# Kernel optimization log

Hardware: AMD Instinct MI355X
Metric: run time of the kernel (lower is better)

Reference implementation:

```python
import jax, jax.numpy as jnp
import numpy as np

B, V, CIN, H, W = 2, 4, 256, 96, 96
COUT, VS = 32, 64


def setup_inputs() -> dict:
    key = jax.random.key(0)
    k1, k2, k3, k4, k5 = jax.random.split(key, 5)
    features = jax.random.normal(k1, (B, V, CIN, H, W), dtype=jnp.float32)
    proj_matricies = jax.random.normal(k2, (B, V, 3, 4), dtype=jnp.float32)
    coord_volumes = jax.random.normal(k3, (B, VS, VS, VS, 3), dtype=jnp.float32) * 1000.0
    W_proc = jax.random.normal(k4, (COUT, CIN), dtype=jnp.float32) * 0.05
    b_proc = jax.random.normal(k5, (COUT,), dtype=jnp.float32) * 0.01
    return {"features": features, "proj_matricies": proj_matricies,
            "coord_volumes": coord_volumes, "W_proc": W_proc, "b_proc": b_proc}


def _bilinear_sample(feat, x, y):
    # feat: [C, H, W]; x, y: [N] pixel coords (align_corners=True mapping already applied)
    Hh, Ww = feat.shape[1], feat.shape[2]
    x0 = jnp.floor(x).astype(jnp.int32); x1 = x0 + 1
    y0 = jnp.floor(y).astype(jnp.int32); y1 = y0 + 1
    wx1 = x - x0; wx0 = 1.0 - wx1
    wy1 = y - y0; wy0 = 1.0 - wy1

    def gather(xi, yi):
        valid = ((xi >= 0) & (xi < Ww) & (yi >= 0) & (yi < Hh)).astype(feat.dtype)
        xc = jnp.clip(xi, 0, Ww - 1); yc = jnp.clip(yi, 0, Hh - 1)
        return feat[:, yc, xc] * valid  # [C, N] (zeros padding)

    return (gather(x0, y0) * (wx0 * wy0)
            + gather(x1, y0) * (wx1 * wy0)
            + gather(x0, y1) * (wx0 * wy1)
            + gather(x1, y1) * (wx1 * wy1))


def reference(features, proj_matricies, coord_volumes, W_proc, b_proc):
    b, v, cin, h, w = features.shape
    vs = coord_volumes.shape[1]
    # 1x1 conv (process_feature)
    feats = jnp.einsum('bvchw,oc->bvohw', features, W_proc) + b_proc[None, None, :, None, None]
    c = feats.shape[2]
    # homogeneous 3D grid points: [B, N, 4]
    pts = coord_volumes.reshape(b, -1, 3)
    pts_h = jnp.concatenate([pts, jnp.ones(pts.shape[:-1] + (1,), pts.dtype)], axis=-1)
    # project to image plane: [B, V, N, 3] homogeneous (u, v, w)
    proj_pts = jnp.einsum('bvij,bnj->bvni', proj_matricies, pts_h)
    wz = proj_pts[..., 2]
    invalid = wz <= 0.0
    wz_safe = jnp.where(wz == 0.0, 1.0, wz)
    u = proj_pts[..., 0] / wz_safe
    ve = proj_pts[..., 1] / wz_safe
    # normalized grid coords (faithful to original: x divided by feature_shape[0]=H, y by feature_shape[1]=W)
    gx = 2.0 * (u / h - 0.5)
    gy = 2.0 * (ve / w - 0.5)
    # align_corners=True pixel coords: x indexes width, y indexes height
    px = (gx + 1.0) * 0.5 * (w - 1)
    py = (gy + 1.0) * 0.5 * (h - 1)
    # sample per (batch, view): [B, V, C, N]
    sampled = jax.vmap(jax.vmap(_bilinear_sample))(feats, px, py)
    sampled = jnp.where(invalid[:, :, None, :], 0.0, sampled)
    # softmax over views per (b, c, voxel), weighted sum
    weights = jax.nn.softmax(sampled, axis=1)
    vol = jnp.sum(sampled * weights, axis=1)  # [B, C, N]
    return vol.reshape(b, c, vs, vs, vs)
```

## Files before the change

kernel.cpp:

```cpp
#include <hip/hip_runtime.h>
#include <hip/hip_bf16.h>

#define CIN   256
#define COUT  32
#define IMG_H 96
#define IMG_W 96
#define HW    (IMG_H*IMG_W)
#define NB    2
#define NV    4
#define VSZ   64
#define NVOX  (VSZ*VSZ*VSZ)

typedef __attribute__((ext_vector_type(2))) float f32x2;

__device__ __forceinline__ float fast_exp2(float x) {
    float r;
    asm("v_exp_f32 %0, %1" : "=v"(r) : "v"(x));
    return r;
}

__global__ __launch_bounds__(512) void conv1x1_kernel(
    const float* __restrict__ features,
    const float* __restrict__ Wp,
    const float* __restrict__ bp,
    __hip_bfloat16* __restrict__ out)
{
    __shared__ float red[2][COUT][128];
    const int wid  = threadIdx.x >> 6;
    const int pxs  = __builtin_amdgcn_readfirstlane(wid & 1);
    const int og   = __builtin_amdgcn_readfirstlane((wid >> 1) & 1);
    const int kh   = __builtin_amdgcn_readfirstlane(wid >> 2);
    const int lane = threadIdx.x & 63;
    const int pxl  = pxs*64 + lane;
    const int bv   = blockIdx.y;
    const int px   = blockIdx.x*128 + pxl;
    const float* f     = features + (size_t)bv*CIN*HW + (size_t)kh*128*HW + px;
    const float* wbase = Wp + (size_t)og*16*CIN + kh*128;

    float acc[16];
    #pragma unroll
    for (int j = 0; j < 16; ++j) acc[j] = 0.f;

    for (int cc = 0; cc < 128; cc += 8) {
        float x[8];
        #pragma unroll
        for (int i = 0; i < 8; ++i)
            x[i] = f[(size_t)(cc + i)*HW];
        #pragma unroll
        for (int i = 0; i < 8; ++i) {
            #pragma unroll
            for (int j = 0; j < 16; ++j)
                acc[j] += x[i] * wbase[(size_t)j*CIN + cc + i];
        }
    }

    #pragma unroll
    for (int j = 0; j < 16; ++j)
        red[kh][og*16 + j][pxl] = acc[j];
    __syncthreads();

    if (kh == 0) {
        union { uint4 u4[2]; __hip_bfloat16 hh[16]; } pk;
        #pragma unroll
        for (int j = 0; j < 16; ++j) {
            const int ch = og*16 + j;
            pk.hh[j] = __float2bfloat16(red[0][ch][pxl] + red[1][ch][pxl] + bp[ch]);
        }
        __hip_bfloat16* op = out + (size_t)(bv*HW + px)*COUT + og*16;
        *(uint4*)(op)     = pk.u4[0];
        *(uint4*)(op + 8) = pk.u4[1];
    }
}

__global__ __launch_bounds__(256, 4) void volgen_kernel(
    const __hip_bfloat16* __restrict__ feats,
    const float* __restrict__ proj,
    const float* __restrict__ coords,
    float* __restrict__ out)
{
    const int tid = threadIdx.x;
    const int b   = blockIdx.y;
    const int n   = blockIdx.x*256 + tid;

    const float* cp = coords + ((size_t)b*NVOX + n)*3;
    const float X = cp[0], Y = cp[1], Z = cp[2];

    const float LOG2E = 1.4426950408889634f;

    int   off[NV][4];
    float wgt[NV][4];
    #pragma unroll
    for (int v = 0; v < NV; ++v) {
        const float* P = proj + (size_t)(b*NV + v)*12;
        const float wz = P[8]*X + P[9]*Y + P[10]*Z + P[11];
        const bool  vz = wz > 0.f;
        const float rz = __builtin_amdgcn_rcpf(wz);
        float px = (P[0]*X + P[1]*Y + P[2]*Z + P[3]) * rz * (95.f/96.f);
        float py = (P[4]*X + P[5]*Y + P[6]*Z + P[7]) * rz * (95.f/96.f);
        px = vz ? px : 0.f;  py = vz ? py : 0.f;
        px = fminf(fmaxf(px, -1.0e6f), 1.0e6f);
        py = fminf(fmaxf(py, -1.0e6f), 1.0e6f);
        const float fx0 = floorf(px), fy0 = floorf(py);
        const int x0 = (int)fx0, y0 = (int)fy0, x1 = x0+1, y1 = y0+1;
        const float wx1 = px - fx0, wx0 = 1.f - wx1;
        const float wy1 = py - fy0, wy0 = 1.f - wy1;
        const bool vx0 = (unsigned)x0 < (unsigned)IMG_W;
        const bool vx1 = (unsigned)x1 < (unsigned)IMG_W;
        const bool vy0 = (unsigned)y0 < (unsigned)IMG_H;
        const bool vy1 = (unsigned)y1 < (unsigned)IMG_H;
        const int cx0 = min(max(x0, 0), IMG_W-1), cx1 = min(max(x1, 0), IMG_W-1);
        const int cy0 = min(max(y0, 0), IMG_H-1), cy1 = min(max(y1, 0), IMG_H-1);
        const int base = ((b*NV + v)*HW)*COUT*2;
        off[v][0] = base + (cy0*IMG_W + cx0)*(COUT*2);  wgt[v][0] = (vz & vx0 & vy0) ? wx0*wy0*LOG2E : 0.f;
        off[v][1] = base + (cy0*IMG_W + cx1)*(COUT*2);  wgt[v][1] = (vz & vx1 & vy0) ? wx1*wy0*LOG2E : 0.f;
        off[v][2] = base + (cy1*IMG_W + cx0)*(COUT*2);  wgt[v][2] = (vz & vx0 & vy1) ? wx0*wy1*LOG2E : 0.f;
        off[v][3] = base + (cy1*IMG_W + cx1)*(COUT*2);  wgt[v][3] = (vz & vx1 & vy1) ? wx1*wy1*LOG2E : 0.f;
    }

    const char* fb = (const char*)feats;
    const size_t ob = (size_t)b*COUT*NVOX + n;
    const float LN2 = 0.6931471805599453f;

    for (int ch0 = 0; ch0 < COUT; ch0 += 8) {
        f32x2 A2[4], B2[4];
        uint4 t[4], tn[4];

        #pragma unroll
        for (int c = 0; c < 4; ++c)
            t[c] = *(const uint4*)(fb + off[0][c] + ch0*2);

        #pragma unroll
        for (int v = 0; v < NV; ++v) {
            if (v < NV-1) {
                #pragma unroll
                for (int c = 0; c < 4; ++c)
                    tn[c] = *(const uint4*)(fb + off[v+1][c] + ch0*2);
            }

            f32x2 s2[4];
            #pragma unroll
            for (int c = 0; c < 4; ++c) {
                const float w = wgt[v][c];
                const f32x2 w2 = { w, w };
                const unsigned tu[4] = { t[c].x, t[c].y, t[c].z, t[c].w };
                #pragma unroll
                for (int k = 0; k < 4; ++k) {
                    f32x2 f2;
                    f2.x = __uint_as_float(tu[k] << 16);
                    f2.y = __uint_as_float(tu[k] & 0xffff0000u);
                    if (c == 0) s2[k] = w2 * f2;
                    else        s2[k] += w2 * f2;
                }
            }

            #pragma unroll
            for (int k = 0; k < 4; ++k) {
                f32x2 e2;
                e2.x = fast_exp2(s2[k].x);
                e2.y = fast_exp2(s2[k].y);
                if (v == 0) { A2[k] = e2;  B2[k] = s2[k]*e2; }
                else        { A2[k] += e2; B2[k] += s2[k]*e2; }
            }

            if (v < NV-1) {
                #pragma unroll
                for (int c = 0; c < 4; ++c) t[c] = tn[c];
            }
        }

        #pragma unroll
        for (int k = 0; k < 4; ++k) {
            out[ob + (size_t)(ch0 + 2*k    )*NVOX] = B2[k].x * __builtin_amdgcn_rcpf(A2[k].x) * LN2;
            out[ob + (size_t)(ch0 + 2*k + 1)*NVOX] = B2[k].y * __builtin_amdgcn_rcpf(A2[k].y) * LN2;
        }
    }
}

extern "C" void kernel_launch(void* const* d_in, const int* in_sizes, int n_in,
                              void* d_out, int out_size, void* d_ws, size_t ws_size,
                              hipStream_t stream)
{
    const float* features = (const float*)d_in[0];
    const float* proj     = (const float*)d_in[1];
    const float* coords   = (const float*)d_in[2];
    const float* Wp       = (const float*)d_in[3];
    const float* bp       = (const float*)d_in[4];
    float* out = (float*)d_out;
    __hip_bfloat16* featsT = (__hip_bfloat16*)d_ws;

    hipLaunchKernelGGL(conv1x1_kernel, dim3(HW/128, NB*NV), dim3(512), 0, stream,
                       features, Wp, bp, featsT);
    hipLaunchKernelGGL(volgen_kernel, dim3(NVOX/256, NB), dim3(256), 0, stream,
                       featsT, proj, coords, out);
}
```

Before: 179.8 us.

## Double-buffer conv1x1 input tiles in LDS via async global-to-LDS loads

```diff
diff --git a/kernel.cpp b/kernel.cpp
--- a/kernel.cpp
+++ b/kernel.cpp
@@ -10,6 +10,7 @@
 #define NV    4
 #define VSZ   64
 #define NVOX  (VSZ*VSZ*VSZ)
+#define TCH   32
 
 typedef __attribute__((ext_vector_type(2))) float f32x2;
 
@@ -19,57 +20,63 @@
     return r;
 }
 
-__global__ __launch_bounds__(512) void conv1x1_kernel(
+__device__ __forceinline__ void gload_lds16(const float* g, float* l) {
+    __builtin_amdgcn_global_load_lds(
+        (const __attribute__((address_space(1))) void*)g,
+        (__attribute__((address_space(3))) void*)l, 16, 0, 0);
+}
+
+__global__ __launch_bounds__(128, 4) void conv1x1_kernel(
     const float* __restrict__ features,
     const float* __restrict__ Wp,
     const float* __restrict__ bp,
     __hip_bfloat16* __restrict__ out)
 {
-    __shared__ float red[2][COUT][128];
-    const int wid  = threadIdx.x >> 6;
-    const int pxs  = __builtin_amdgcn_readfirstlane(wid & 1);
-    const int og   = __builtin_amdgcn_readfirstlane((wid >> 1) & 1);
-    const int kh   = __builtin_amdgcn_readfirstlane(wid >> 2);
+    __shared__ float tile[2][TCH][64];
+    const int og   = __builtin_amdgcn_readfirstlane((threadIdx.x >> 6) & 1);
     const int lane = threadIdx.x & 63;
-    const int pxl  = pxs*64 + lane;
     const int bv   = blockIdx.y;
-    const int px   = blockIdx.x*128 + pxl;
-    const float* f     = features + (size_t)bv*CIN*HW + (size_t)kh*128*HW + px;
-    const float* wbase = Wp + (size_t)og*16*CIN + kh*128;
+    const int px0  = blockIdx.x*64;
+    const float* fb    = features + (size_t)bv*CIN*HW + px0;
+    const float* wbase = Wp + (size_t)og*16*CIN;
+
+    #pragma unroll
+    for (int i = 0; i < 4; ++i)
+        gload_lds16(fb + (size_t)(og*16 + i*4 + (lane>>4))*HW + (lane&15)*4,
+                    &tile[0][og*16 + i*4][0]);
+    __syncthreads();
 
     float acc[16];
     #pragma unroll
     for (int j = 0; j < 16; ++j) acc[j] = 0.f;
 
-    for (int cc = 0; cc < 128; cc += 8) {
-        float x[8];
-        #pragma unroll
-        for (int i = 0; i < 8; ++i)
-            x[i] = f[(size_t)(cc + i)*HW];
-        #pragma unroll
-        for (int i = 0; i < 8; ++i) {
+    #pragma unroll
+    for (int t = 0; t < CIN/TCH; ++t) {
+        const int cur = t & 1;
+        if (t + 1 < CIN/TCH) {
+            #pragma unroll
+            for (int i = 0; i < 4; ++i)
+                gload_lds16(fb + (size_t)((t+1)*TCH + og*16 + i*4 + (lane>>4))*HW
+                               + (lane&15)*4,
+                            &tile[cur^1][og*16 + i*4][0]);
+        }
+        #pragma unroll
+        for (int c = 0; c < TCH; ++c) {
+            const float x = tile[cur][c][lane];
             #pragma unroll
             for (int j = 0; j < 16; ++j)
-                acc[j] += x[i] * wbase[(size_t)j*CIN + cc + i];
-        }
+                acc[j] += x * wbase[(size_t)j*CIN + t*TCH + c];
+        }
+        __syncthreads();
     }
 
+    union { uint4 u4[2]; __hip_bfloat16 h[16]; } pk;
     #pragma unroll
     for (int j = 0; j < 16; ++j)
-        red[kh][og*16 + j][pxl] = acc[j];
-    __syncthreads();
-
-    if (kh == 0) {
-        union { uint4 u4[2]; __hip_bfloat16 hh[16]; } pk;
-        #pragma unroll
-        for (int j = 0; j < 16; ++j) {
-            const int ch = og*16 + j;
-            pk.hh[j] = __float2bfloat16(red[0][ch][pxl] + red[1][ch][pxl] + bp[ch]);
-        }
-        __hip_bfloat16* op = out + (size_t)(bv*HW + px)*COUT + og*16;
-        *(uint4*)(op)     = pk.u4[0];
-        *(uint4*)(op + 8) = pk.u4[1];
-    }
+        pk.h[j] = __float2bfloat16(acc[j] + bp[og*16 + j]);
+    __hip_bfloat16* op = out + ((size_t)(bv*HW + px0 + lane))*COUT + og*16;
+    *(uint4*)(op)     = pk.u4[0];
+    *(uint4*)(op + 8) = pk.u4[1];
 }
 
 __global__ __launch_bounds__(256, 4) void volgen_kernel(
@@ -188,7 +195,7 @@
     float* out = (float*)d_out;
     __hip_bfloat16* featsT = (__hip_bfloat16*)d_ws;
 
-    hipLaunchKernelGGL(conv1x1_kernel, dim3(HW/128, NB*NV), dim3(512), 0, stream,
+    hipLaunchKernelGGL(conv1x1_kernel, dim3(HW/64, NB*NV), dim3(128), 0, stream,
                        features, Wp, bp, featsT);
     hipLaunchKernelGGL(volgen_kernel, dim3(NVOX/256, NB), dim3(256), 0, stream,
                        featsT, proj, coords, out);
```

Measured after the change: 316.4 us. 1.76x slower.
